# Optimization experiments

Hardware: AMD Instinct MI355X
Metric: run time of the kernel (lower is better)

## Reference

```python
import jax, jax.numpy as jnp
import numpy as np

NEG_SLOPE = 0.2  # PyG GATConv LeakyReLU slope


def _gat_conv(x, ei, W, a_src, a_dst, bias, concat):
    # x: [N, F_in], ei: [2, E] (with self-loops), W: [F_in, H*C], a_*: [H, C]
    N = x.shape[0]
    H, C = a_src.shape
    xp = (x @ W).reshape(N, H, C)                       # [N, H, C]
    src, dst = ei[0], ei[1]
    s_score = jnp.einsum('nhc,hc->nh', xp, a_src)       # [N, H]
    d_score = jnp.einsum('nhc,hc->nh', xp, a_dst)       # [N, H]
    e = jax.nn.leaky_relu(s_score[src] + d_score[dst], negative_slope=NEG_SLOPE)  # [E, H]
    # segment softmax over incoming edges of each dst node
    m = jax.ops.segment_max(e, dst, num_segments=N)     # [N, H]
    ex = jnp.exp(e - m[dst])                            # [E, H]
    den = jax.ops.segment_sum(ex, dst, num_segments=N)  # [N, H]
    alpha = ex / den[dst]                               # [E, H]
    msg = alpha[:, :, None] * xp[src]                   # [E, H, C]
    out = jax.ops.segment_sum(msg, dst, num_segments=N) # [N, H, C]
    out = out.reshape(N, H * C) if concat else out.mean(axis=1)
    return out + bias


def _add_self_loops(edge_index, num_nodes):
    ar = jnp.arange(num_nodes, dtype=edge_index.dtype)
    return jnp.concatenate([edge_index, jnp.stack([ar, ar])], axis=1)


def setup_inputs() -> dict:
    key = jax.random.key(0)
    ks = jax.random.split(key, 16)
    N, E, F_in, Hd, heads, out_c, G = 50000, 800000, 128, 64, 4, 10, 64
    x = jax.random.normal(ks[0], (N, F_in), dtype=jnp.float32)
    edge_index = jax.random.randint(ks[1], (2, E), 0, N, dtype=jnp.int64)
    batch = jnp.sort(jax.random.randint(ks[2], (N,), 0, G, dtype=jnp.int64))
    sc = lambda f: 1.0 / np.sqrt(f)
    # layer 1: in -> hidden, heads=4, concat
    W1 = jax.random.normal(ks[3], (F_in, heads * Hd), dtype=jnp.float32) * sc(F_in)
    a_src1 = jax.random.normal(ks[4], (heads, Hd), dtype=jnp.float32) * sc(Hd)
    a_dst1 = jax.random.normal(ks[5], (heads, Hd), dtype=jnp.float32) * sc(Hd)
    b1 = jnp.zeros((heads * Hd,), dtype=jnp.float32)
    # layer 2: heads*hidden -> hidden, heads=1, concat=False
    W2 = jax.random.normal(ks[6], (heads * Hd, Hd), dtype=jnp.float32) * sc(heads * Hd)
    a_src2 = jax.random.normal(ks[7], (1, Hd), dtype=jnp.float32) * sc(Hd)
    a_dst2 = jax.random.normal(ks[8], (1, Hd), dtype=jnp.float32) * sc(Hd)
    b2 = jnp.zeros((Hd,), dtype=jnp.float32)
    # final linear
    Wl = jax.random.normal(ks[9], (Hd, out_c), dtype=jnp.float32) * sc(Hd)
    bl = jnp.zeros((out_c,), dtype=jnp.float32)
    return {"x": x, "edge_index": edge_index, "batch": batch,
            "W1": W1, "a_src1": a_src1, "a_dst1": a_dst1, "b1": b1,
            "W2": W2, "a_src2": a_src2, "a_dst2": a_dst2, "b2": b2,
            "Wl": Wl, "bl": bl}


def reference(x, edge_index, batch, W1, a_src1, a_dst1, b1,
              W2, a_src2, a_dst2, b2, Wl, bl):
    N = x.shape[0]
    G = 64  # number of graphs
    ei = _add_self_loops(edge_index, N)
    h = jax.nn.elu(_gat_conv(x, ei, W1, a_src1, a_dst1, b1, concat=True))
    h = jax.nn.elu(_gat_conv(h, ei, W2, a_src2, a_dst2, b2, concat=False))
    # global mean pool over graphs
    sums = jax.ops.segment_sum(h, batch, num_segments=G)            # [G, Hd]
    cnt = jax.ops.segment_sum(jnp.ones((N,), h.dtype), batch, num_segments=G)
    pooled = sums / jnp.maximum(cnt, 1.0)[:, None]
    return pooled @ Wl + bl
```

## Files before the change

### kernel.cpp

```cpp
#include <hip/hip_runtime.h>
#include <hip/hip_bf16.h>
#include <cstdint>

#define NN   50000
#define NE   800000
#define NET  850000
#define FIN  128
#define FH1  256
#define HD   64
#define NG   64
#define OUTC 10
#define NBS  ((NN + 255) / 256)

typedef __attribute__((ext_vector_type(8))) short short8v;
typedef __attribute__((ext_vector_type(4))) float f32x4;

__device__ __forceinline__ float bf2f(unsigned short u) {
    union { unsigned int i; float f; } v; v.i = ((unsigned int)u) << 16; return v.f;
}
__device__ __forceinline__ float bflo(unsigned int u) {
    union { unsigned int i; float f; } v; v.i = u << 16; return v.f;
}
__device__ __forceinline__ float bfhi(unsigned int u) {
    union { unsigned int i; float f; } v; v.i = u & 0xFFFF0000u; return v.f;
}
__device__ __forceinline__ unsigned short f2bf(float f) {
    union { float fl; unsigned int i; } v; v.fl = f;
    unsigned int x = v.i;
    return (unsigned short)((x + 0x7FFFu + ((x >> 16) & 1u)) >> 16);
}
__device__ __forceinline__ float leakyr(float v) { return v > 0.f ? v : 0.2f * v; }
__device__ __forceinline__ float elu1(float v)  { return v > 0.f ? v : expm1f(v); }

__global__ __launch_bounds__(256) void k_gemm1(
    const float* __restrict__ x, const float* __restrict__ W1,
    const float* __restrict__ asrc, const float* __restrict__ adst,
    unsigned short* __restrict__ xp1, float* __restrict__ s1t, float* __restrict__ d1)
{
    __shared__ __align__(16) short Ash[64 * 40];
    __shared__ __align__(16) short Bsh[64 * 40];
    int row0 = blockIdx.x * 64;
    int head = blockIdx.y;
    int n0   = head * 64;
    int tid  = threadIdx.x;
    int wv   = tid >> 6;
    int lane = tid & 63;
    int g    = lane >> 4;
    int c    = lane & 15;

    f32x4 acc[4] = {{0,0,0,0},{0,0,0,0},{0,0,0,0},{0,0,0,0}};

    int sr = tid >> 2;
    int sq = tid & 3;

    for (int k0 = 0; k0 < FIN; k0 += 32) {
        {
            int gr = row0 + sr;
            float4 v0 = make_float4(0,0,0,0), v1 = make_float4(0,0,0,0);
            if (gr < NN) {
                const float4* p = reinterpret_cast<const float4*>(x + (size_t)gr * FIN + k0 + sq * 8);
                v0 = p[0]; v1 = p[1];
            }
            short8v pk;
            pk[0] = (short)f2bf(v0.x); pk[1] = (short)f2bf(v0.y);
            pk[2] = (short)f2bf(v0.z); pk[3] = (short)f2bf(v0.w);
            pk[4] = (short)f2bf(v1.x); pk[5] = (short)f2bf(v1.y);
            pk[6] = (short)f2bf(v1.z); pk[7] = (short)f2bf(v1.w);
            *reinterpret_cast<short8v*>(&Ash[sr * 40 + sq * 8]) = pk;
        }
        {
            int n  = tid & 63;
            int kg = tid >> 6;
            short8v pk;
            #pragma unroll
            for (int i = 0; i < 8; i++)
                pk[i] = (short)f2bf(W1[(size_t)(k0 + kg * 8 + i) * FH1 + n0 + n]);
            *reinterpret_cast<short8v*>(&Bsh[n * 40 + kg * 8]) = pk;
        }
        __syncthreads();
        short8v af = *reinterpret_cast<const short8v*>(&Ash[(16 * wv + c) * 40 + g * 8]);
        #pragma unroll
        for (int j = 0; j < 4; j++) {
            short8v bf = *reinterpret_cast<const short8v*>(&Bsh[(16 * j + c) * 40 + g * 8]);
            acc[j] = __builtin_amdgcn_mfma_f32_16x16x32_bf16(af, bf, acc[j], 0, 0, 0);
        }
        __syncthreads();
    }

    float as[4], ad[4];
    #pragma unroll
    for (int j = 0; j < 4; j++) {
        as[j] = asrc[n0 + 16 * j + c];
        ad[j] = adst[n0 + 16 * j + c];
    }
    #pragma unroll
    for (int r = 0; r < 4; r++) {
        int row = row0 + 16 * wv + 4 * g + r;
        float sv = 0.f, dv = 0.f;
        #pragma unroll
        for (int j = 0; j < 4; j++) {
            float v = acc[j][r];
            sv = fmaf(v, as[j], sv);
            dv = fmaf(v, ad[j], dv);
            if (row < NN) xp1[(size_t)row * FH1 + n0 + 16 * j + c] = f2bf(v);
        }
        #pragma unroll
        for (int off = 8; off >= 1; off >>= 1) {
            sv += __shfl_xor(sv, off, 16);
            dv += __shfl_xor(dv, off, 16);
        }
        if (c == 0 && row < NN) {
            s1t[(size_t)head * NN + row] = sv;
            d1[row * 4 + head] = dv;
        }
    }
}

__global__ __launch_bounds__(256) void k_hist(
    const int* __restrict__ ei, int* __restrict__ deg)
{
    int e = blockIdx.x * 256 + threadIdx.x;
    if (e >= NET) return;
    int dst = (e < NE) ? ei[NE + e] : (e - NE);
    atomicAdd(&deg[dst], 1);
}

__global__ __launch_bounds__(256) void k_scan_a(
    const int* __restrict__ deg, int* __restrict__ part)
{
    __shared__ int sm[256];
    int t = threadIdx.x;
    int idx = blockIdx.x * 256 + t;
    sm[t] = (idx < NN) ? deg[idx] : 0;
    __syncthreads();
    for (int off = 128; off >= 1; off >>= 1) {
        if (t < off) sm[t] += sm[t + off];
        __syncthreads();
    }
    if (t == 0) part[blockIdx.x] = sm[0];
}

__global__ __launch_bounds__(256) void k_scan_b(
    int* __restrict__ part, int* __restrict__ rowptr)
{
    __shared__ int sm[256];
    int t = threadIdx.x;
    int v = (t < NBS) ? part[t] : 0;
    sm[t] = v;
    __syncthreads();
    for (int off = 1; off < 256; off <<= 1) {
        int u = (t >= off) ? sm[t - off] : 0;
        __syncthreads();
        sm[t] += u;
        __syncthreads();
    }
    if (t < NBS) part[t] = sm[t] - v;
    if (t == 0) rowptr[NN] = NET;
}

__global__ __launch_bounds__(256) void k_scan_c(
    const int* __restrict__ deg, const int* __restrict__ part,
    int* __restrict__ rowptr)
{
    __shared__ int sm[256];
    int t = threadIdx.x;
    int idx = blockIdx.x * 256 + t;
    int v = (idx < NN) ? deg[idx] : 0;
    sm[t] = v;
    __syncthreads();
    for (int off = 1; off < 256; off <<= 1) {
        int u = (t >= off) ? sm[t - off] : 0;
        __syncthreads();
        sm[t] += u;
        __syncthreads();
    }
    if (idx < NN) rowptr[idx] = part[blockIdx.x] + sm[t] - v;
}

__global__ __launch_bounds__(256) void k_scatter(
    const int* __restrict__ ei, const int* __restrict__ rowptr,
    int* __restrict__ cursor, int* __restrict__ eidx)
{
    int e = blockIdx.x * 256 + threadIdx.x;
    if (e >= NET) return;
    int src, dst;
    if (e < NE) { src = ei[e]; dst = ei[NE + e]; }
    else        { src = dst = e - NE; }
    int pos = atomicAdd(&cursor[dst], 1);
    eidx[rowptr[dst] + pos] = src;
}

__global__ __launch_bounds__(256) void k_pull1(
    const int* __restrict__ rowptr, const int* __restrict__ eidx,
    const float* __restrict__ s1t, const float* __restrict__ d1,
    const unsigned short* __restrict__ xp1, const float* __restrict__ b1,
    unsigned short* __restrict__ h1)
{
    int wv = threadIdx.x >> 6;
    int lane = threadIdx.x & 63;
    int n = blockIdx.x * 4 + wv;
    if (n >= NN) return;
    int head = lane >> 4;
    int c0 = lane * 4;
    int hNN = head * NN;
    float dv = d1[(size_t)n * 4 + head];
    int jb = __builtin_amdgcn_readfirstlane(rowptr[n]);
    int je = __builtin_amdgcn_readfirstlane(rowptr[n + 1]);
    float a0 = 0.f, a1 = 0.f, a2 = 0.f, a3 = 0.f;
    float den = 0.f;
    int j = jb;
    for (; j + 8 <= je; j += 8) {
        int s[8];
        #pragma unroll
        for (int q = 0; q < 8; q++) s[q] = eidx[j + q];
        float sc[8];
        uint2 u[8];
        #pragma unroll
        for (int q = 0; q < 8; q++) {
            const float* srow = s1t + s[q];
            sc[q] = srow[hNN];
            const unsigned short* xrow = xp1 + (size_t)s[q] * FH1;
            u[q] = *reinterpret_cast<const uint2*>(xrow + c0);
        }
        #pragma unroll
        for (int q = 0; q < 8; q++) {
            float ex = __expf(leakyr(sc[q] + dv));
            a0 = fmaf(bflo(u[q].x), ex, a0);
            a1 = fmaf(bfhi(u[q].x), ex, a1);
            a2 = fmaf(bflo(u[q].y), ex, a2);
            a3 = fmaf(bfhi(u[q].y), ex, a3);
            den += ex;
        }
    }
    for (; j < je; j++) {
        int src = eidx[j];
        const float* srow = s1t + src;
        float ex = __expf(leakyr(srow[hNN] + dv));
        const unsigned short* xrow = xp1 + (size_t)src * FH1;
        uint2 u = *reinterpret_cast<const uint2*>(xrow + c0);
        a0 = fmaf(bflo(u.x), ex, a0);
        a1 = fmaf(bfhi(u.x), ex, a1);
        a2 = fmaf(bflo(u.y), ex, a2);
        a3 = fmaf(bfhi(u.y), ex, a3);
        den += ex;
    }
    float inv = 1.0f / den;
    float4 b = *reinterpret_cast<const float4*>(b1 + c0);
    ushort4 st;
    st.x = f2bf(elu1(fmaf(a0, inv, b.x)));
    st.y = f2bf(elu1(fmaf(a1, inv, b.y)));
    st.z = f2bf(elu1(fmaf(a2, inv, b.z)));
    st.w = f2bf(elu1(fmaf(a3, inv, b.w)));
    *reinterpret_cast<ushort4*>(h1 + (size_t)n * FH1 + c0) = st;
}

__global__ __launch_bounds__(256) void k_gemm2(
    const unsigned short* __restrict__ h1, const float* __restrict__ W2,
    const float* __restrict__ asrc2, const float* __restrict__ adst2,
    unsigned short* __restrict__ xp2, float* __restrict__ s2, float* __restrict__ d2)
{
    __shared__ __align__(16) short Ash[64 * 40];
    __shared__ __align__(16) short Bsh[64 * 40];
    int row0 = blockIdx.x * 64;
    int tid  = threadIdx.x;
    int wv   = tid >> 6;
    int lane = tid & 63;
    int g    = lane >> 4;
    int c    = lane & 15;

    f32x4 acc[4] = {{0,0,0,0},{0,0,0,0},{0,0,0,0},{0,0,0,0}};

    int sr = tid >> 2;
    int sq = tid & 3;

    for (int k0 = 0; k0 < FH1; k0 += 32) {
        {
            int gr = row0 + sr;
            uint4 v = make_uint4(0, 0, 0, 0);
            if (gr < NN) v = *reinterpret_cast<const uint4*>(h1 + (size_t)gr * FH1 + k0 + sq * 8);
            *reinterpret_cast<uint4*>(&Ash[sr * 40 + sq * 8]) = v;
        }
        {
            int n  = tid & 63;
            int kg = tid >> 6;
            short8v pk;
            #pragma unroll
            for (int i = 0; i < 8; i++)
                pk[i] = (short)f2bf(W2[(size_t)(k0 + kg * 8 + i) * HD + n]);
            *reinterpret_cast<short8v*>(&Bsh[n * 40 + kg * 8]) = pk;
        }
        __syncthreads();
        short8v af = *reinterpret_cast<const short8v*>(&Ash[(16 * wv + c) * 40 + g * 8]);
        #pragma unroll
        for (int j = 0; j < 4; j++) {
            short8v bf = *reinterpret_cast<const short8v*>(&Bsh[(16 * j + c) * 40 + g * 8]);
            acc[j] = __builtin_amdgcn_mfma_f32_16x16x32_bf16(af, bf, acc[j], 0, 0, 0);
        }
        __syncthreads();
    }

    float as[4], ad[4];
    #pragma unroll
    for (int j = 0; j < 4; j++) {
        as[j] = asrc2[16 * j + c];
        ad[j] = adst2[16 * j + c];
    }
    #pragma unroll
    for (int r = 0; r < 4; r++) {
        int row = row0 + 16 * wv + 4 * g + r;
        float sv = 0.f, dv = 0.f;
        #pragma unroll
        for (int j = 0; j < 4; j++) {
            float v = acc[j][r];
            sv = fmaf(v, as[j], sv);
            dv = fmaf(v, ad[j], dv);
            if (row < NN) xp2[(size_t)row * HD + 16 * j + c] = f2bf(v);
        }
        #pragma unroll
        for (int off = 8; off >= 1; off >>= 1) {
            sv += __shfl_xor(sv, off, 16);
            dv += __shfl_xor(dv, off, 16);
        }
        if (c == 0 && row < NN) { s2[row] = sv; d2[row] = dv; }
    }
}

__global__ __launch_bounds__(256) void k_pull2(
    const int* __restrict__ rowptr, const int* __restrict__ eidx,
    const float* __restrict__ s2, const float* __restrict__ d2,
    const unsigned short* __restrict__ xp2, const float* __restrict__ b2,
    float* __restrict__ h2)
{
    int wv = threadIdx.x >> 6;
    int lane = threadIdx.x & 63;
    int n = blockIdx.x * 4 + wv;
    if (n >= NN) return;
    int half = lane >> 5;
    int c = lane & 31;
    float dv = d2[n];
    int jb = __builtin_amdgcn_readfirstlane(rowptr[n]);
    int je = __builtin_amdgcn_readfirstlane(rowptr[n + 1]);
    float a0 = 0.f, a1 = 0.f, den = 0.f;
    int j = jb;
    for (; j + 16 <= je; j += 16) {
        #pragma unroll
        for (int p = 0; p < 8; p++) {
            int e = j + 2 * p + half;
            int src = eidx[e];
            float sc = s2[src];
            unsigned int u = *reinterpret_cast<const unsigned int*>(xp2 + (size_t)src * HD + 2 * c);
            float ex = __expf(leakyr(sc + dv));
            a0 = fmaf(bflo(u), ex, a0);
            a1 = fmaf(bfhi(u), ex, a1);
            den += ex;
        }
    }
    for (; j < je; j += 2) {
        int e = j + half;
        bool valid = e < je;
        int ec = valid ? e : (je - 1);
        int src = eidx[ec];
        float sc = s2[src];
        unsigned int u = *reinterpret_cast<const unsigned int*>(xp2 + (size_t)src * HD + 2 * c);
        float ex = valid ? __expf(leakyr(sc + dv)) : 0.f;
        a0 = fmaf(bflo(u), ex, a0);
        a1 = fmaf(bfhi(u), ex, a1);
        den += ex;
    }
    a0 += __shfl_xor(a0, 32);
    a1 += __shfl_xor(a1, 32);
    den += __shfl_xor(den, 32);
    if (half == 0) {
        float inv = 1.0f / den;
        float2 bb = *reinterpret_cast<const float2*>(b2 + 2 * c);
        float2 o;
        o.x = elu1(fmaf(a0, inv, bb.x));
        o.y = elu1(fmaf(a1, inv, bb.y));
        *reinterpret_cast<float2*>(h2 + (size_t)n * HD + 2 * c) = o;
    }
}

__global__ __launch_bounds__(256) void k_pool(
    const float* __restrict__ h2, const int* __restrict__ batch,
    float* __restrict__ pooled)
{
    int g = blockIdx.x;
    int lo = 0, hi = NN;
    while (lo < hi) { int m = (lo + hi) >> 1; if (batch[m] < g) lo = m + 1; else hi = m; }
    int start = lo;
    hi = NN;
    while (lo < hi) { int m = (lo + hi) >> 1; if (batch[m] < g + 1) lo = m + 1; else hi = m; }
    int end = lo;
    int c = threadIdx.x & 63;
    int rg = threadIdx.x >> 6;
    float sum = 0.f;
    for (int n = start + rg; n < end; n += 4)
        sum += h2[(size_t)n * HD + c];
    __shared__ float red[4][64];
    red[rg][c] = sum;
    __syncthreads();
    if (threadIdx.x < 64) {
        float tot = red[0][c] + red[1][c] + red[2][c] + red[3][c];
        float cnt = (float)(end - start);
        pooled[g * HD + c] = tot / fmaxf(cnt, 1.f);
    }
}

__global__ __launch_bounds__(256) void k_final(
    const float* __restrict__ pooled, const float* __restrict__ Wl,
    const float* __restrict__ bl, float* __restrict__ out)
{
    int t = blockIdx.x * 256 + threadIdx.x;
    if (t >= NG * OUTC) return;
    int g = t / OUTC, o = t % OUTC;
    float acc = bl[o];
    #pragma unroll
    for (int k = 0; k < HD; k++)
        acc = fmaf(pooled[g * HD + k], Wl[k * OUTC + o], acc);
    out[t] = acc;
}

extern "C" void kernel_launch(void* const* d_in, const int* in_sizes, int n_in,
                              void* d_out, int out_size, void* d_ws, size_t ws_size,
                              hipStream_t stream) {
    const float* x     = (const float*)d_in[0];
    const int*   ei    = (const int*)d_in[1];
    const int*   batch = (const int*)d_in[2];
    const float* W1    = (const float*)d_in[3];
    const float* as1   = (const float*)d_in[4];
    const float* ad1   = (const float*)d_in[5];
    const float* b1    = (const float*)d_in[6];
    const float* W2    = (const float*)d_in[7];
    const float* as2   = (const float*)d_in[8];
    const float* ad2   = (const float*)d_in[9];
    const float* b2    = (const float*)d_in[10];
    const float* Wl    = (const float*)d_in[11];
    const float* bl    = (const float*)d_in[12];
    float* out = (float*)d_out;

    char* w = (char*)d_ws;
    size_t off = 0;
    auto alloc = [&](size_t bytes) {
        void* p = (void*)(w + off);
        off = (off + bytes + 255) & ~(size_t)255;
        return p;
    };
    int* deg    = (int*)alloc((size_t)NN * 4);
    int* cursor = (int*)alloc((size_t)NN * 4);
    size_t zbytes = off;
    int* part   = (int*)alloc((size_t)NBS * 4);
    int* rowptr = (int*)alloc((size_t)(NN + 1) * 4);
    int* eidx   = (int*)alloc((size_t)NET * 4);
    unsigned short* xp1 = (unsigned short*)alloc((size_t)NN * FH1 * 2);
    unsigned short* h1  = (unsigned short*)alloc((size_t)NN * FH1 * 2);
    float* s1t = (float*)alloc((size_t)NN * 4 * 4);
    float* d1s = (float*)alloc((size_t)NN * 4 * 4);
    unsigned short* xp2 = (unsigned short*)alloc((size_t)NN * HD * 2);
    float* s2  = (float*)alloc((size_t)NN * 4);
    float* d2s = (float*)alloc((size_t)NN * 4);
    float* h2  = (float*)alloc((size_t)NN * HD * 4);
    float* pooled = (float*)alloc((size_t)NG * HD * 4);

    hipMemsetAsync(d_ws, 0, zbytes, stream);

    k_hist   <<<(NET + 255) / 256, 256, 0, stream>>>(ei, deg);
    k_scan_a <<<NBS, 256, 0, stream>>>(deg, part);
    k_scan_b <<<1, 256, 0, stream>>>(part, rowptr);
    k_scan_c <<<NBS, 256, 0, stream>>>(deg, part, rowptr);
    k_scatter<<<(NET + 255) / 256, 256, 0, stream>>>(ei, rowptr, cursor, eidx);

    dim3 g1((NN + 63) / 64, 4);
    k_gemm1<<<g1, 256, 0, stream>>>(x, W1, as1, ad1, xp1, s1t, d1s);
    k_pull1<<<(NN + 3) / 4, 256, 0, stream>>>(rowptr, eidx, s1t, d1s, xp1, b1, h1);
    k_gemm2<<<(NN + 63) / 64, 256, 0, stream>>>(h1, W2, as2, ad2, xp2, s2, d2s);
    k_pull2<<<(NN + 3) / 4, 256, 0, stream>>>(rowptr, eidx, s2, d2s, xp2, b2, h2);
    k_pool <<<NG, 256, 0, stream>>>(h2, batch, pooled);
    k_final<<<(NG * OUTC + 255) / 256, 256, 0, stream>>>(pooled, Wl, bl, out);
}
```

Measured before the change: 287.7 us.

## Compute all heads per block in gemm1 and split pooling across slices with atomics

The layer-1 GEMM now has each block compute all four heads for its 64 rows, so x is loaded and converted to bf16 once instead of four times. Each wave owns one head and keeps a 4x4 grid of MFMA accumulators. Global mean pooling is split into 8 slices per graph that atomically add into a zeroed buffer, and the division by node count moves into the final linear kernel. This raises register pressure in gemm1 and makes the pooled sums depend on the order of the atomic adds.

```diff
diff --git a/kernel.cpp b/kernel.cpp
--- a/kernel.cpp
+++ b/kernel.cpp
@@ -38,17 +38,19 @@
     unsigned short* __restrict__ xp1, float* __restrict__ s1t, float* __restrict__ d1)
 {
     __shared__ __align__(16) short Ash[64 * 40];
-    __shared__ __align__(16) short Bsh[64 * 40];
+    __shared__ __align__(16) short Bsh[256 * 40];
     int row0 = blockIdx.x * 64;
-    int head = blockIdx.y;
-    int n0   = head * 64;
     int tid  = threadIdx.x;
     int wv   = tid >> 6;
     int lane = tid & 63;
     int g    = lane >> 4;
     int c    = lane & 15;
 
-    f32x4 acc[4] = {{0,0,0,0},{0,0,0,0},{0,0,0,0},{0,0,0,0}};
+    f32x4 acc[4][4];
+    #pragma unroll
+    for (int i = 0; i < 4; i++)
+        #pragma unroll
+        for (int j = 0; j < 4; j++) acc[i][j] = (f32x4){0.f, 0.f, 0.f, 0.f};
 
     int sr = tid >> 2;
     int sq = tid & 3;
@@ -69,24 +71,31 @@
             *reinterpret_cast<short8v*>(&Ash[sr * 40 + sq * 8]) = pk;
         }
         {
-            int n  = tid & 63;
-            int kg = tid >> 6;
-            short8v pk;
             #pragma unroll
-            for (int i = 0; i < 8; i++)
-                pk[i] = (short)f2bf(W1[(size_t)(k0 + kg * 8 + i) * FH1 + n0 + n]);
-            *reinterpret_cast<short8v*>(&Bsh[n * 40 + kg * 8]) = pk;
-        }
-        __syncthreads();
-        short8v af = *reinterpret_cast<const short8v*>(&Ash[(16 * wv + c) * 40 + g * 8]);
-        #pragma unroll
-        for (int j = 0; j < 4; j++) {
-            short8v bf = *reinterpret_cast<const short8v*>(&Bsh[(16 * j + c) * 40 + g * 8]);
-            acc[j] = __builtin_amdgcn_mfma_f32_16x16x32_bf16(af, bf, acc[j], 0, 0, 0);
-        }
-        __syncthreads();
-    }
-
+            for (int kg = 0; kg < 4; kg++) {
+                short8v pk;
+                #pragma unroll
+                for (int i = 0; i < 8; i++)
+                    pk[i] = (short)f2bf(W1[(size_t)(k0 + kg * 8 + i) * FH1 + tid]);
+                *reinterpret_cast<short8v*>(&Bsh[tid * 40 + kg * 8]) = pk;
+            }
+        }
+        __syncthreads();
+        short8v bf[4];
+        #pragma unroll
+        for (int j = 0; j < 4; j++)
+            bf[j] = *reinterpret_cast<const short8v*>(&Bsh[(64 * wv + 16 * j + c) * 40 + g * 8]);
+        #pragma unroll
+        for (int rt = 0; rt < 4; rt++) {
+            short8v af = *reinterpret_cast<const short8v*>(&Ash[(16 * rt + c) * 40 + g * 8]);
+            #pragma unroll
+            for (int j = 0; j < 4; j++)
+                acc[rt][j] = __builtin_amdgcn_mfma_f32_16x16x32_bf16(af, bf[j], acc[rt][j], 0, 0, 0);
+        }
+        __syncthreads();
+    }
+
+    int n0 = 64 * wv;
     float as[4], ad[4];
     #pragma unroll
     for (int j = 0; j < 4; j++) {
@@ -94,24 +103,27 @@
         ad[j] = adst[n0 + 16 * j + c];
     }
     #pragma unroll
-    for (int r = 0; r < 4; r++) {
-        int row = row0 + 16 * wv + 4 * g + r;
-        float sv = 0.f, dv = 0.f;
-        #pragma unroll
-        for (int j = 0; j < 4; j++) {
-            float v = acc[j][r];
-            sv = fmaf(v, as[j], sv);
-            dv = fmaf(v, ad[j], dv);
-            if (row < NN) xp1[(size_t)row * FH1 + n0 + 16 * j + c] = f2bf(v);
-        }
-        #pragma unroll
-        for (int off = 8; off >= 1; off >>= 1) {
-            sv += __shfl_xor(sv, off, 16);
-            dv += __shfl_xor(dv, off, 16);
-        }
-        if (c == 0 && row < NN) {
-            s1t[(size_t)head * NN + row] = sv;
-            d1[row * 4 + head] = dv;
+    for (int rt = 0; rt < 4; rt++) {
+        #pragma unroll
+        for (int r = 0; r < 4; r++) {
+            int row = row0 + 16 * rt + 4 * g + r;
+            float sv = 0.f, dv = 0.f;
+            #pragma unroll
+            for (int j = 0; j < 4; j++) {
+                float v = acc[rt][j][r];
+                sv = fmaf(v, as[j], sv);
+                dv = fmaf(v, ad[j], dv);
+                if (row < NN) xp1[(size_t)row * FH1 + n0 + 16 * j + c] = f2bf(v);
+            }
+            #pragma unroll
+            for (int off = 8; off >= 1; off >>= 1) {
+                sv += __shfl_xor(sv, off, 16);
+                dv += __shfl_xor(dv, off, 16);
+            }
+            if (c == 0 && row < NN) {
+                s1t[(size_t)wv * NN + row] = sv;
+                d1[row * 4 + wv] = dv;
+            }
         }
     }
 }
@@ -382,42 +394,53 @@
 
 __global__ __launch_bounds__(256) void k_pool(
     const float* __restrict__ h2, const int* __restrict__ batch,
-    float* __restrict__ pooled)
+    float* __restrict__ pooled )
 {
     int g = blockIdx.x;
+    int sslice = blockIdx.y;
     int lo = 0, hi = NN;
     while (lo < hi) { int m = (lo + hi) >> 1; if (batch[m] < g) lo = m + 1; else hi = m; }
     int start = lo;
     hi = NN;
     while (lo < hi) { int m = (lo + hi) >> 1; if (batch[m] < g + 1) lo = m + 1; else hi = m; }
     int end = lo;
+    int len = end - start;
+    int chunk = (len + 7) >> 3;
+    int b0 = start + sslice * chunk;
+    int b1 = min(b0 + chunk, end);
     int c = threadIdx.x & 63;
     int rg = threadIdx.x >> 6;
     float sum = 0.f;
-    for (int n = start + rg; n < end; n += 4)
+    for (int n = b0 + rg; n < b1; n += 4)
         sum += h2[(size_t)n * HD + c];
     __shared__ float red[4][64];
     red[rg][c] = sum;
     __syncthreads();
     if (threadIdx.x < 64) {
         float tot = red[0][c] + red[1][c] + red[2][c] + red[3][c];
-        float cnt = (float)(end - start);
-        pooled[g * HD + c] = tot / fmaxf(cnt, 1.f);
+        if (tot != 0.f) atomicAdd(&pooled[g * HD + c], tot);
     }
 }
 
 __global__ __launch_bounds__(256) void k_final(
-    const float* __restrict__ pooled, const float* __restrict__ Wl,
-    const float* __restrict__ bl, float* __restrict__ out)
+    const float* __restrict__ pooled, const int* __restrict__ batch,
+    const float* __restrict__ Wl, const float* __restrict__ bl,
+    float* __restrict__ out)
 {
     int t = blockIdx.x * 256 + threadIdx.x;
     if (t >= NG * OUTC) return;
     int g = t / OUTC, o = t % OUTC;
-    float acc = bl[o];
+    int lo = 0, hi = NN;
+    while (lo < hi) { int m = (lo + hi) >> 1; if (batch[m] < g) lo = m + 1; else hi = m; }
+    int start = lo;
+    hi = NN;
+    while (lo < hi) { int m = (lo + hi) >> 1; if (batch[m] < g + 1) lo = m + 1; else hi = m; }
+    float cnt = (float)(lo - start);
+    float acc = 0.f;
     #pragma unroll
     for (int k = 0; k < HD; k++)
         acc = fmaf(pooled[g * HD + k], Wl[k * OUTC + o], acc);
-    out[t] = acc;
+    out[t] = acc / fmaxf(cnt, 1.f) + bl[o];
 }
 
 extern "C" void kernel_launch(void* const* d_in, const int* in_sizes, int n_in,
@@ -447,6 +470,7 @@
     };
     int* deg    = (int*)alloc((size_t)NN * 4);
     int* cursor = (int*)alloc((size_t)NN * 4);
+    float* pooled = (float*)alloc((size_t)NG * HD * 4);
     size_t zbytes = off;
     int* part   = (int*)alloc((size_t)NBS * 4);
     int* rowptr = (int*)alloc((size_t)(NN + 1) * 4);
@@ -459,7 +483,6 @@
     float* s2  = (float*)alloc((size_t)NN * 4);
     float* d2s = (float*)alloc((size_t)NN * 4);
     float* h2  = (float*)alloc((size_t)NN * HD * 4);
-    float* pooled = (float*)alloc((size_t)NG * HD * 4);
 
     hipMemsetAsync(d_ws, 0, zbytes, stream);
 
@@ -469,11 +492,11 @@
     k_scan_c <<<NBS, 256, 0, stream>>>(deg, part, rowptr);
     k_scatter<<<(NET + 255) / 256, 256, 0, stream>>>(ei, rowptr, cursor, eidx);
 
-    dim3 g1((NN + 63) / 64, 4);
-    k_gemm1<<<g1, 256, 0, stream>>>(x, W1, as1, ad1, xp1, s1t, d1s);
+    k_gemm1<<<(NN + 63) / 64, 256, 0, stream>>>(x, W1, as1, ad1, xp1, s1t, d1s);
     k_pull1<<<(NN + 3) / 4, 256, 0, stream>>>(rowptr, eidx, s1t, d1s, xp1, b1, h1);
     k_gemm2<<<(NN + 63) / 64, 256, 0, stream>>>(h1, W2, as2, ad2, xp2, s2, d2s);
     k_pull2<<<(NN + 3) / 4, 256, 0, stream>>>(rowptr, eidx, s2, d2s, xp2, b2, h2);
-    k_pool <<<NG, 256, 0, stream>>>(h2, batch, pooled);
-    k_final<<<(NG * OUTC + 255) / 256, 256, 0, stream>>>(pooled, Wl, bl, out);
-}
+    dim3 gp(NG, 8);
+    k_pool <<<gp, 256, 0, stream>>>(h2, batch, pooled);
+    k_final<<<(NG * OUTC + 255) / 256, 256, 0, stream>>>(pooled, batch, Wl, bl, out);
+}
```

New measurement: 257.2 us, median of 2. 10.6% less time.
